# Kernel tuning notes

Measured on AMD Instinct MI355X. Metric: run time of the kernel, lower is better.

## Reference

```python
import jax, jax.numpy as jnp
import numpy as np

NEG = -10000.0

def _wn(W, g):
    # weight_norm with dim=None: single scalar g scaling W / ||W||_F
    return g * W / jnp.linalg.norm(W)

def setup_inputs() -> dict:
    key = jax.random.key(0)
    ks = jax.random.split(key, 10)
    B, N, H, P = 128, 4096, 128, 128
    v = jax.random.normal(ks[0], (B, N, H), jnp.float32)
    q = jax.random.normal(ks[1], (B, H), jnp.float32)
    mask = jnp.ones((B, N), jnp.float32)
    # params (out_dim, in_dim) like torch Linear
    Wv = jax.random.normal(ks[2], (P, H), jnp.float32) / np.sqrt(H)
    bv = jnp.zeros((P,), jnp.float32)
    gv = jnp.float32(jnp.linalg.norm(Wv))
    Wq = jax.random.normal(ks[3], (P, H), jnp.float32) / np.sqrt(H)
    bq = jnp.zeros((P,), jnp.float32)
    gq = jnp.float32(jnp.linalg.norm(Wq))
    Wa = jax.random.normal(ks[4], (1, P), jnp.float32) / np.sqrt(P)
    ba = jnp.zeros((1,), jnp.float32)
    ga = jnp.float32(jnp.linalg.norm(Wa))
    return {"v": v, "q": q, "mask": mask, "Wv": Wv, "bv": bv, "gv": gv,
            "Wq": Wq, "bq": bq, "gq": gq, "Wa": Wa, "ba": ba, "ga": ga}

def reference(v, q, mask, Wv, bv, gv, Wq, bq, gq, Wa, ba, ga):
    # FCNet projections (dropout is identity at inference; FCNet applies no relu)
    v_proj = jnp.einsum('bnh,ph->bnp', v, _wn(Wv, gv)) + bv        # [B,N,P]
    q_proj = (q @ _wn(Wq, gq).T + bq)[:, None, :]                   # [B,1,P]
    h = jax.nn.relu(v_proj + q_proj)                                # [B,N,P]
    logits = jnp.einsum('bnp,p->bn', h, _wn(Wa, ga)[0]) + ba[0]     # [B,N]
    logits = logits + (1.0 - mask) * NEG
    w = jax.nn.softmax(logits, axis=-1)                             # [B,N]
    w_att = w[:, :, None]                                           # [B,N,1]
    att = jnp.sum(v * w_att, axis=1)                                # [B,H]
    return att, w_att
```

## Files before the change

kernel.cpp:

```cpp
#include <hip/hip_runtime.h>

typedef _Float16 half8_t __attribute__((ext_vector_type(8)));
typedef float f32x4 __attribute__((ext_vector_type(4)));

#define B_ 128
#define N_ 4096
#define H_ 128
#define P_ 128
#define CCH 8
#define ROWS_PER_CHUNK (N_ / CCH)
#define TILES (ROWS_PER_CHUNK / 64)

#define OFF_SCALES 0
#define OFF_WA     16
#define OFF_QPC    256
#define OFF_BPACK  16640
#define OFF_LOGITS 24832
#define OFF_PART   549120
#define OFF_FIN    819456

__device__ __forceinline__ float block_reduce_sum(float val, float* red, int tid) {
    red[tid] = val;
    __syncthreads();
    for (int s = 128; s > 0; s >>= 1) {
        if (tid < s) red[tid] += red[tid + s];
        __syncthreads();
    }
    float r = red[0];
    __syncthreads();
    return r;
}

__global__ __launch_bounds__(256) void k0a_prep(
    const float* __restrict__ Wv, const float* __restrict__ gv,
    const float* __restrict__ Wq, const float* __restrict__ gq,
    const float* __restrict__ Wa, const float* __restrict__ ga,
    float* __restrict__ ws)
{
    __shared__ float red[256];
    __shared__ float s_sv, s_sa;
    const int tid = threadIdx.x;

    float sv2 = 0.f, sq2 = 0.f, sa2 = 0.f;
    for (int i = tid; i < P_ * H_; i += 256) {
        float x = Wv[i]; sv2 += x * x;
        float y = Wq[i]; sq2 += y * y;
    }
    if (tid < P_) { float z = Wa[tid]; sa2 = z * z; }

    float nv2 = block_reduce_sum(sv2, red, tid);
    float nq2 = block_reduce_sum(sq2, red, tid);
    float na2 = block_reduce_sum(sa2, red, tid);

    if (tid == 0) {
        float sv = gv[0] / sqrtf(nv2);
        float sq = gq[0] / sqrtf(nq2);
        float sa = ga[0] / sqrtf(na2);
        ws[OFF_SCALES + 0] = sv;
        ws[OFF_SCALES + 1] = sq;
        ws[OFF_SCALES + 2] = sa;
        s_sv = sv; s_sa = sa;
    }
    __syncthreads();

    const float sv = s_sv, sa = s_sa;
    _Float16* bp = (_Float16*)(ws + OFF_BPACK);
    for (int s = tid; s < 16384; s += 256) {
        int j  = s & 7;
        int L  = (s >> 3) & 63;
        int pt = (s >> 9) & 7;
        int kk = s >> 12;
        int p = pt * 16 + (L & 15);
        int h = kk * 32 + (L >> 4) * 8 + j;
        bp[s] = (_Float16)(Wv[p * H_ + h] * sv);
    }
    if (tid < P_) ws[OFF_WA + tid] = Wa[tid] * sa;
}

__global__ __launch_bounds__(128) void k0b_qproj(
    const float* __restrict__ q, const float* __restrict__ Wq,
    const float* __restrict__ bq, const float* __restrict__ bv,
    float* __restrict__ ws)
{
    const int b = blockIdx.x, p = threadIdx.x;
    const float sq = ws[OFF_SCALES + 1];
    const float* qr = q + b * H_;
    const float* wr = Wq + p * H_;
    float acc = 0.f;
#pragma unroll 8
    for (int h = 0; h < H_; ++h) acc += qr[h] * wr[h];
    ws[OFF_QPC + b * P_ + p] = acc * sq + bq[p] + bv[p];
}

__global__ __launch_bounds__(256) void k1_main(
    const float* __restrict__ v, const float* __restrict__ mask,
    const float* __restrict__ ba, float* __restrict__ ws)
{
    const int c = blockIdx.x;
    const int b = blockIdx.y;
    const int tid = threadIdx.x;
    const int lane = tid & 63;
    const int w = tid >> 6;

    __shared__ __align__(16) _Float16 Bl[16384];
    __shared__ float qpcs[P_];
    __shared__ float was[P_];
    __shared__ float smask[ROWS_PER_CHUNK];
    __shared__ float obuf[4][P_];
    __shared__ float mbuf[4], lbuf[4];

    {
        const uint4* src = (const uint4*)(ws + OFF_BPACK);
        uint4* dst = (uint4*)Bl;
#pragma unroll
        for (int i = 0; i < 8; ++i) dst[tid + i * 256] = src[tid + i * 256];
        if (tid < P_) {
            qpcs[tid] = ws[OFF_QPC + b * P_ + tid];
            was[tid]  = ws[OFF_WA + tid];
        }
#pragma unroll
        for (int i = 0; i < ROWS_PER_CHUNK / 256; ++i)
            smask[tid + i * 256] = mask[(size_t)b * N_ + c * ROWS_PER_CHUNK + tid + i * 256];
    }
    const float ba0 = ba[0];
    __syncthreads();

    const int rloc = lane & 15;
    const int grp  = lane >> 4;
    const int colb = grp * 8;

    float m_w = -1e30f, l_w = 0.f;
    float o32[32];
#pragma unroll
    for (int j = 0; j < 32; ++j) o32[j] = 0.f;

    for (int it = 0; it < TILES; ++it) {
        const int r0 = it * 64 + w * 16;
        const int n0w = c * ROWS_PER_CHUNK + r0;

        const float* vrow = v + ((size_t)b * N_ + n0w + rloc) * H_;
        half8_t af[4];
#pragma unroll
        for (int kk = 0; kk < 4; ++kk) {
            const float4* p4 = (const float4*)(vrow + kk * 32 + colb);
            float4 f0 = p4[0], f1 = p4[1];
            half8_t a;
            a[0] = (_Float16)f0.x; a[1] = (_Float16)f0.y;
            a[2] = (_Float16)f0.z; a[3] = (_Float16)f0.w;
            a[4] = (_Float16)f1.x; a[5] = (_Float16)f1.y;
            a[6] = (_Float16)f1.z; a[7] = (_Float16)f1.w;
            af[kk] = a;
        }

        float lp[4];
        lp[0] = lp[1] = lp[2] = lp[3] = 0.f;
#pragma unroll
        for (int pt = 0; pt < 8; ++pt) {
            const int p = pt * 16 + rloc;
            const float qv = qpcs[p];
            f32x4 acc = {qv, qv, qv, qv};
#pragma unroll
            for (int kk = 0; kk < 4; ++kk) {
                half8_t bf = *(const half8_t*)&Bl[(((kk * 8 + pt) * 64) + lane) * 8];
                acc = __builtin_amdgcn_mfma_f32_16x16x32_f16(af[kk], bf, acc, 0, 0, 0);
            }
            const float wv = was[p];
#pragma unroll
            for (int r = 0; r < 4; ++r)
                lp[r] += fmaxf(acc[r], 0.f) * wv;
        }
#pragma unroll
        for (int m = 1; m <= 8; m <<= 1) {
#pragma unroll
            for (int r = 0; r < 4; ++r) lp[r] += __shfl_xor(lp[r], m, 64);
        }
#pragma unroll
        for (int r = 0; r < 4; ++r) {
            const float mk = smask[r0 + grp * 4 + r];
            lp[r] += ba0 + (1.0f - mk) * (-10000.0f);
        }

        const int srcl = (rloc >> 2) << 4;
        float t0 = __shfl(lp[0], srcl, 64);
        float t1 = __shfl(lp[1], srcl, 64);
        float t2 = __shfl(lp[2], srcl, 64);
        float t3 = __shfl(lp[3], srcl, 64);
        float a01 = (rloc & 1) ? t1 : t0;
        float a23 = (rloc & 1) ? t3 : t2;
        float lg_me = (rloc & 2) ? a23 : a01;

        if (lane < 16) ws[OFF_LOGITS + (size_t)b * N_ + n0w + lane] = lg_me;

        float mt = fmaxf(fmaxf(lp[0], lp[1]), fmaxf(lp[2], lp[3]));
        mt = fmaxf(mt, __shfl_xor(mt, 16, 64));
        mt = fmaxf(mt, __shfl_xor(mt, 32, 64));

        const float mn = fmaxf(m_w, mt);
        const float alpha = __expf(m_w - mn);
        const float wme = __expf(lg_me - mn);
        float s = wme;
#pragma unroll
        for (int m = 1; m <= 8; m <<= 1) s += __shfl_xor(s, m, 64);
        l_w = l_w * alpha + s;
        m_w = mn;

        if (alpha != 1.0f) {
#pragma unroll
            for (int j = 0; j < 32; ++j) o32[j] *= alpha;
        }
#pragma unroll
        for (int kk = 0; kk < 4; ++kk) {
#pragma unroll
            for (int j = 0; j < 8; ++j)
                o32[kk * 8 + j] += wme * (float)af[kk][j];
        }
    }

#pragma unroll
    for (int m = 1; m <= 8; m <<= 1) {
#pragma unroll
        for (int j = 0; j < 32; ++j) o32[j] += __shfl_xor(o32[j], m, 64);
    }
    {
        const int j0 = rloc * 2;
#pragma unroll
        for (int u = 0; u < 2; ++u) {
            const int j = j0 + u;
            obuf[w][(j >> 3) * 32 + colb + (j & 7)] = o32[j];
        }
        if (lane == 0) { mbuf[w] = m_w; lbuf[w] = l_w; }
    }
    __syncthreads();

    float* part = ws + OFF_PART + ((size_t)b * CCH + c) * 132;
    if (tid < P_) {
        const float mb = fmaxf(fmaxf(mbuf[0], mbuf[1]), fmaxf(mbuf[2], mbuf[3]));
        float lb = 0.f, oh = 0.f;
#pragma unroll
        for (int ww = 0; ww < 4; ++ww) {
            const float e = __expf(mbuf[ww] - mb);
            lb += e * lbuf[ww];
            oh += e * obuf[ww][tid];
        }
        part[2 + tid] = oh;
        if (tid == 0) { part[0] = mb; part[1] = lb; }
    }
}

__global__ __launch_bounds__(128) void k2a_combine(
    float* __restrict__ ws, float* __restrict__ out)
{
    const int b = blockIdx.x, h = threadIdx.x;
    const float* part = ws + OFF_PART + (size_t)b * CCH * 132;
    float m = -1e30f;
#pragma unroll
    for (int c = 0; c < CCH; ++c) m = fmaxf(m, part[c * 132]);
    float l = 0.f, a = 0.f;
#pragma unroll
    for (int c = 0; c < CCH; ++c) {
        const float e = __expf(part[c * 132] - m);
        l += e * part[c * 132 + 1];
        a += e * part[c * 132 + 2 + h];
    }
    out[b * H_ + h] = a / l;
    if (h == 0) {
        ws[OFF_FIN + b] = m;
        ws[OFF_FIN + B_ + b] = 1.0f / l;
    }
}

__global__ __launch_bounds__(256) void k2b_weights(
    const float* __restrict__ ws, float* __restrict__ out)
{
    const int idx = blockIdx.x * 256 + threadIdx.x;
    const int b = idx >> 12;
    const float lg = ws[OFF_LOGITS + idx];
    out[B_ * H_ + idx] = __expf(lg - ws[OFF_FIN + b]) * ws[OFF_FIN + B_ + b];
}

extern "C" void kernel_launch(void* const* d_in, const int* in_sizes, int n_in,
                              void* d_out, int out_size, void* d_ws, size_t ws_size,
                              hipStream_t stream) {
    const float* v    = (const float*)d_in[0];
    const float* q    = (const float*)d_in[1];
    const float* mask = (const float*)d_in[2];
    const float* Wv   = (const float*)d_in[3];
    const float* bv   = (const float*)d_in[4];
    const float* gv   = (const float*)d_in[5];
    const float* Wq   = (const float*)d_in[6];
    const float* bq   = (const float*)d_in[7];
    const float* gq   = (const float*)d_in[8];
    const float* Wa   = (const float*)d_in[9];
    const float* ba   = (const float*)d_in[10];
    const float* ga   = (const float*)d_in[11];
    float* out = (float*)d_out;
    float* ws  = (float*)d_ws;

    k0a_prep<<<1, 256, 0, stream>>>(Wv, gv, Wq, gq, Wa, ga, ws);
    k0b_qproj<<<B_, 128, 0, stream>>>(q, Wq, bq, bv, ws);
    k1_main<<<dim3(CCH, B_), 256, 0, stream>>>(v, mask, ba, ws);
    k2a_combine<<<B_, 128, 0, stream>>>(ws, out);
    k2b_weights<<<(B_ * N_) / 256, 256, 0, stream>>>(ws, out);
}
```

Before: 436.6 us.

## Fuse q-projection into main kernel and merge combine/weights kernels

Computes the q projection inside each main-kernel block instead of in a separate kernel. The combine and softmax-weight kernels are merged into one kernel that recomputes the max and sum per block. The prep kernel now uses 1024 threads with wave shuffle reductions. The aim is to cut launch count and serialization overhead, at the price of redundant qproj and combine arithmetic per block.

Result: faster. 407.3 us (-6.7%).

```diff
diff --git a/kernel.cpp b/kernel.cpp
--- a/kernel.cpp
+++ b/kernel.cpp
@@ -13,49 +13,49 @@
 
 #define OFF_SCALES 0
 #define OFF_WA     16
-#define OFF_QPC    256
 #define OFF_BPACK  16640
 #define OFF_LOGITS 24832
 #define OFF_PART   549120
-#define OFF_FIN    819456
-
-__device__ __forceinline__ float block_reduce_sum(float val, float* red, int tid) {
-    red[tid] = val;
-    __syncthreads();
-    for (int s = 128; s > 0; s >>= 1) {
-        if (tid < s) red[tid] += red[tid + s];
-        __syncthreads();
-    }
-    float r = red[0];
-    __syncthreads();
-    return r;
-}
-
-__global__ __launch_bounds__(256) void k0a_prep(
+
+__global__ __launch_bounds__(1024) void k0_prep(
     const float* __restrict__ Wv, const float* __restrict__ gv,
     const float* __restrict__ Wq, const float* __restrict__ gq,
     const float* __restrict__ Wa, const float* __restrict__ ga,
     float* __restrict__ ws)
 {
-    __shared__ float red[256];
+    const int tid  = threadIdx.x;
+    const int lane = tid & 63;
+    const int w    = tid >> 6;
+
+    float sv2 = 0.f, sq2 = 0.f, sa2 = 0.f;
+    const float4* Wv4 = (const float4*)Wv;
+    const float4* Wq4 = (const float4*)Wq;
+#pragma unroll
+    for (int i = 0; i < 4; ++i) {
+        float4 a = Wv4[tid + i * 1024];
+        sv2 += a.x * a.x + a.y * a.y + a.z * a.z + a.w * a.w;
+        float4 b = Wq4[tid + i * 1024];
+        sq2 += b.x * b.x + b.y * b.y + b.z * b.z + b.w * b.w;
+    }
+    if (tid < P_) { float z = Wa[tid]; sa2 = z * z; }
+
+#pragma unroll
+    for (int m = 1; m <= 32; m <<= 1) {
+        sv2 += __shfl_xor(sv2, m, 64);
+        sq2 += __shfl_xor(sq2, m, 64);
+        sa2 += __shfl_xor(sa2, m, 64);
+    }
+    __shared__ float rv[16], rq[16], ra[16];
     __shared__ float s_sv, s_sa;
-    const int tid = threadIdx.x;
-
-    float sv2 = 0.f, sq2 = 0.f, sa2 = 0.f;
-    for (int i = tid; i < P_ * H_; i += 256) {
-        float x = Wv[i]; sv2 += x * x;
-        float y = Wq[i]; sq2 += y * y;
-    }
-    if (tid < P_) { float z = Wa[tid]; sa2 = z * z; }
-
-    float nv2 = block_reduce_sum(sv2, red, tid);
-    float nq2 = block_reduce_sum(sq2, red, tid);
-    float na2 = block_reduce_sum(sa2, red, tid);
-
+    if (lane == 0) { rv[w] = sv2; rq[w] = sq2; ra[w] = sa2; }
+    __syncthreads();
     if (tid == 0) {
-        float sv = gv[0] / sqrtf(nv2);
-        float sq = gq[0] / sqrtf(nq2);
-        float sa = ga[0] / sqrtf(na2);
+        float nv = 0.f, nq = 0.f, na = 0.f;
+#pragma unroll
+        for (int i = 0; i < 16; ++i) { nv += rv[i]; nq += rq[i]; na += ra[i]; }
+        float sv = gv[0] / sqrtf(nv);
+        float sq = gq[0] / sqrtf(nq);
+        float sa = ga[0] / sqrtf(na);
         ws[OFF_SCALES + 0] = sv;
         ws[OFF_SCALES + 1] = sq;
         ws[OFF_SCALES + 2] = sa;
@@ -65,7 +65,9 @@
 
     const float sv = s_sv, sa = s_sa;
     _Float16* bp = (_Float16*)(ws + OFF_BPACK);
-    for (int s = tid; s < 16384; s += 256) {
+#pragma unroll
+    for (int k = 0; k < 16; ++k) {
+        int s  = tid + k * 1024;
         int j  = s & 7;
         int L  = (s >> 3) & 63;
         int pt = (s >> 9) & 7;
@@ -77,24 +79,12 @@
     if (tid < P_) ws[OFF_WA + tid] = Wa[tid] * sa;
 }
 
-__global__ __launch_bounds__(128) void k0b_qproj(
+__global__ __launch_bounds__(256) void k1_main(
+    const float* __restrict__ v, const float* __restrict__ mask,
+    const float* __restrict__ ba,
     const float* __restrict__ q, const float* __restrict__ Wq,
     const float* __restrict__ bq, const float* __restrict__ bv,
     float* __restrict__ ws)
-{
-    const int b = blockIdx.x, p = threadIdx.x;
-    const float sq = ws[OFF_SCALES + 1];
-    const float* qr = q + b * H_;
-    const float* wr = Wq + p * H_;
-    float acc = 0.f;
-#pragma unroll 8
-    for (int h = 0; h < H_; ++h) acc += qr[h] * wr[h];
-    ws[OFF_QPC + b * P_ + p] = acc * sq + bq[p] + bv[p];
-}
-
-__global__ __launch_bounds__(256) void k1_main(
-    const float* __restrict__ v, const float* __restrict__ mask,
-    const float* __restrict__ ba, float* __restrict__ ws)
 {
     const int c = blockIdx.x;
     const int b = blockIdx.y;
@@ -114,10 +104,22 @@
         uint4* dst = (uint4*)Bl;
 #pragma unroll
         for (int i = 0; i < 8; ++i) dst[tid + i * 256] = src[tid + i * 256];
-        if (tid < P_) {
-            qpcs[tid] = ws[OFF_QPC + b * P_ + tid];
-            was[tid]  = ws[OFF_WA + tid];
-        }
+
+        const int p  = tid >> 1;
+        const int hh = tid & 1;
+        const float sq = ws[OFF_SCALES + 1];
+        const float4* qr = (const float4*)(q + (size_t)b * H_) + hh * 16;
+        const float4* wr = (const float4*)(Wq + (size_t)p * H_) + hh * 16;
+        float acc = 0.f;
+#pragma unroll
+        for (int i = 0; i < 16; ++i) {
+            float4 a = qr[i], cc4 = wr[i];
+            acc += a.x * cc4.x + a.y * cc4.y + a.z * cc4.z + a.w * cc4.w;
+        }
+        acc += __shfl_xor(acc, 1, 64);
+        if (hh == 0) qpcs[p] = acc * sq + bq[p] + bv[p];
+
+        if (tid < P_) was[tid] = ws[OFF_WA + tid];
 #pragma unroll
         for (int i = 0; i < ROWS_PER_CHUNK / 256; ++i)
             smask[tid + i * 256] = mask[(size_t)b * N_ + c * ROWS_PER_CHUNK + tid + i * 256];
@@ -247,35 +249,40 @@
     }
 }
 
-__global__ __launch_bounds__(128) void k2a_combine(
-    float* __restrict__ ws, float* __restrict__ out)
-{
-    const int b = blockIdx.x, h = threadIdx.x;
-    const float* part = ws + OFF_PART + (size_t)b * CCH * 132;
-    float m = -1e30f;
-#pragma unroll
-    for (int c = 0; c < CCH; ++c) m = fmaxf(m, part[c * 132]);
-    float l = 0.f, a = 0.f;
-#pragma unroll
-    for (int c = 0; c < CCH; ++c) {
-        const float e = __expf(part[c * 132] - m);
-        l += e * part[c * 132 + 1];
-        a += e * part[c * 132 + 2 + h];
-    }
-    out[b * H_ + h] = a / l;
-    if (h == 0) {
-        ws[OFF_FIN + b] = m;
-        ws[OFF_FIN + B_ + b] = 1.0f / l;
-    }
-}
-
-__global__ __launch_bounds__(256) void k2b_weights(
+__global__ __launch_bounds__(256) void k2_final(
     const float* __restrict__ ws, float* __restrict__ out)
 {
-    const int idx = blockIdx.x * 256 + threadIdx.x;
-    const int b = idx >> 12;
-    const float lg = ws[OFF_LOGITS + idx];
-    out[B_ * H_ + idx] = __expf(lg - ws[OFF_FIN + b]) * ws[OFF_FIN + B_ + b];
+    const int c4 = blockIdx.x;
+    const int b  = blockIdx.y;
+    const int tid = threadIdx.x;
+    const float* part = ws + OFF_PART + (size_t)b * CCH * 132;
+
+    float m = -1e30f;
+#pragma unroll
+    for (int cc = 0; cc < CCH; ++cc) m = fmaxf(m, part[cc * 132]);
+    float l = 0.f;
+#pragma unroll
+    for (int cc = 0; cc < CCH; ++cc)
+        l += __expf(part[cc * 132] - m) * part[cc * 132 + 1];
+    const float il = 1.0f / l;
+
+    if (c4 == 0 && tid < P_) {
+        float a = 0.f;
+#pragma unroll
+        for (int cc = 0; cc < CCH; ++cc)
+            a += __expf(part[cc * 132] - m) * part[cc * 132 + 2 + tid];
+        out[(size_t)b * H_ + tid] = a * il;
+    }
+
+    const float4* lg4 = (const float4*)(ws + OFF_LOGITS + (size_t)b * N_ + c4 * 1024);
+    float4* w4 = (float4*)(out + B_ * H_ + (size_t)b * N_ + c4 * 1024);
+    float4 g = lg4[tid];
+    float4 r;
+    r.x = __expf(g.x - m) * il;
+    r.y = __expf(g.y - m) * il;
+    r.z = __expf(g.z - m) * il;
+    r.w = __expf(g.w - m) * il;
+    w4[tid] = r;
 }
 
 extern "C" void kernel_launch(void* const* d_in, const int* in_sizes, int n_in,
@@ -296,9 +303,7 @@
     float* out = (float*)d_out;
     float* ws  = (float*)d_ws;
 
-    k0a_prep<<<1, 256, 0, stream>>>(Wv, gv, Wq, gq, Wa, ga, ws);
-    k0b_qproj<<<B_, 128, 0, stream>>>(q, Wq, bq, bv, ws);
-    k1_main<<<dim3(CCH, B_), 256, 0, stream>>>(v, mask, ba, ws);
-    k2a_combine<<<B_, 128, 0, stream>>>(ws, out);
-    k2b_weights<<<(B_ * N_) / 256, 256, 0, stream>>>(ws, out);
+    k0_prep<<<1, 1024, 0, stream>>>(Wv, gv, Wq, gq, Wa, ga, ws);
+    k1_main<<<dim3(CCH, B_), 256, 0, stream>>>(v, mask, ba, q, Wq, bq, bv, ws);
+    k2_final<<<dim3(4, B_), 256, 0, stream>>>(ws, out);
 }
```
